# Performance work log

Hardware: AMD Instinct MI355X
Metric: run time of the kernel (lower is better)

## Reference

```python
import jax, jax.numpy as jnp
import numpy as np

D_K = 32
N_HEADS = 16


def setup_inputs() -> dict:
    key = jax.random.key(0)
    ks = jax.random.split(key, 11)
    B, S, F = 32, 2048, 128
    d_k, d_v, filt = 32, 32, 3
    return {
        "q_in": jax.random.normal(ks[0], (B, S, F), jnp.float32),
        "k_in": jax.random.normal(ks[1], (B, S, F), jnp.float32),
        "v_in": jax.random.normal(ks[2], (B, S, F), jnp.float32),
        "Wq": jax.random.normal(ks[3], (F, d_k), jnp.float32) * 0.05,
        "bq": jax.random.normal(ks[4], (d_k,), jnp.float32) * 0.05,
        "Wk": jax.random.normal(ks[5], (F, d_k), jnp.float32) * 0.05,
        "bk": jax.random.normal(ks[6], (d_k,), jnp.float32) * 0.05,
        "Wv": jax.random.normal(ks[7], (F, d_v), jnp.float32) * 0.05,
        "bv": jax.random.normal(ks[8], (d_v,), jnp.float32) * 0.05,
        "Wo": jax.random.normal(ks[9], (N_HEADS * d_v, filt), jnp.float32) * 0.05,
        "bo": jax.random.normal(ks[10], (filt,), jnp.float32) * 0.05,
    }


def reference(q_in, k_in, v_in, Wq, bq, Wk, bk, Wv, bv, Wo, bo):
    # SingleAttention: Dense projections then scaled dot-product attention.
    q = q_in @ Wq + bq            # [B,S,d_k]
    k = k_in @ Wk + bk            # [B,S,d_k]
    v = v_in @ Wv + bv            # [B,S,d_v]
    scores = jnp.einsum('bqd,bkd->bqk', q, k) / jnp.sqrt(jnp.float32(D_K))
    attn = jax.nn.softmax(scores, axis=-1)
    head = jnp.einsum('bqk,bkd->bqd', attn, v)  # [B,S,d_v]
    # Original uses [SingleAttention()]*n_heads -> all heads are the SAME layer,
    # so the concat is n_heads identical copies of one head output.
    combined = jnp.tile(head, (1, 1, N_HEADS))   # [B,S,n_heads*d_v]
    return combined @ Wo + bo                    # [B,S,filter_size]
```

## Files before the change

### kernel.cpp

```cpp
#include <hip/hip_runtime.h>
#include <stdint.h>

using f16 = _Float16;
typedef _Float16 f16x8 __attribute__((ext_vector_type(8)));
typedef float f32x4 __attribute__((ext_vector_type(4)));

constexpr int Bn    = 32;
constexpr int Sn    = 2048;
constexpr int Fn    = 128;
constexpr int DKn   = 32;
constexpr int NHn   = 16;
constexpr int FILTn = 3;
constexpr int Mn    = Bn * Sn;

constexpr float QSCALE = 0.1767766952966369f * 1.4426950408889634f;

constexpr int MISC_WOEFF = 0;
constexpr int MISC_BO    = 96;
constexpr int MISC_BQ    = 99;
constexpr int MISC_BK    = 131;
constexpr int MISC_BV    = 163;

#define ASYNC_COPY16(gp, lp)                                                   \
    __builtin_amdgcn_global_load_lds(                                          \
        (const __attribute__((address_space(1))) uint32_t*)(const void*)(gp),  \
        (__attribute__((address_space(3))) uint32_t*)(lp), 16, 0, 0)

#define WAIT_VM2 __builtin_amdgcn_s_waitcnt(0xF72)
#define WAIT_VM0 __builtin_amdgcn_s_waitcnt(0xF70)

__global__ __launch_bounds__(256) void prep_kernel(
    const float* __restrict__ Wq, const float* __restrict__ bq,
    const float* __restrict__ Wk, const float* __restrict__ bk,
    const float* __restrict__ Wv, const float* __restrict__ bv,
    const float* __restrict__ Wo, const float* __restrict__ bo,
    f16* __restrict__ wtg, float* __restrict__ misc)
{
    for (int idx = blockIdx.x * 256 + threadIdx.x; idx < 3 * 4096;
         idx += gridDim.x * 256) {
        const int T    = idx >> 12;
        const int r    = idx & 4095;
        const int nt   = r >> 11;
        const int ks   = (r >> 9) & 3;
        const int lane = (r >> 3) & 63;
        const int j    = r & 7;
        const int k    = ks * 32 + (lane >> 4) * 8 + j;
        const int c    = nt * 16 + (lane & 15);
        const float* W = (T == 0) ? Wq : ((T == 1) ? Wk : Wv);
        const float sc = (T == 0) ? QSCALE : 1.0f;
        wtg[idx] = (f16)(W[k * DKn + c] * sc);
    }
    if (blockIdx.x == 0) {
        const int t = threadIdx.x;
        if (t < 96) {
            const int d = t / 3, f = t - 3 * d;
            float s = 0.f;
#pragma unroll
            for (int h = 0; h < NHn; ++h) s += Wo[(h * DKn + d) * FILTn + f];
            misc[MISC_WOEFF + t] = s;
        } else if (t < 99) {
            misc[MISC_BO + (t - 96)] = bo[t - 96];
        } else if (t < 131) {
            misc[MISC_BQ + (t - 99)] = bq[t - 99] * QSCALE;
        } else if (t < 163) {
            misc[MISC_BK + (t - 131)] = bk[t - 131];
        } else if (t < 195) {
            misc[MISC_BV + (t - 163)] = bv[t - 163];
        }
    }
}

__global__ __launch_bounds__(256, 4) void qkv_proj(
    const float* __restrict__ q_in, const float* __restrict__ k_in,
    const float* __restrict__ v_in,
    const f16* __restrict__ wtg, const float* __restrict__ misc,
    f16* __restrict__ q_ws, f16* __restrict__ k_ws, f16* __restrict__ v_ws)
{
    const int t    = threadIdx.x;
    const int w    = t >> 6;
    const int lane = t & 63;
    const int n    = lane & 15;
    const int quad = lane >> 4;
    const int T    = blockIdx.x >> 10;
    const int row0 = ((blockIdx.x & 1023) * 4 + w) * 16;
    const float* in = (T == 0) ? q_in : ((T == 1) ? k_in : v_in);

    f16x8 wf[2][4];
#pragma unroll
    for (int nt = 0; nt < 2; ++nt)
#pragma unroll
        for (int ks = 0; ks < 4; ++ks)
            wf[nt][ks] =
                *(const f16x8*)(wtg + T * 4096 + (nt * 4 + ks) * 512 + lane * 8);

    f16x8 af[4];
#pragma unroll
    for (int ks = 0; ks < 4; ++ks) {
        const float* p  = in + (size_t)(row0 + n) * Fn + ks * 32 + quad * 8;
        const float4 x0 = *(const float4*)p;
        const float4 x1 = *(const float4*)(p + 4);
        f16x8 a;
        a[0]=(f16)x0.x; a[1]=(f16)x0.y; a[2]=(f16)x0.z; a[3]=(f16)x0.w;
        a[4]=(f16)x1.x; a[5]=(f16)x1.y; a[6]=(f16)x1.z; a[7]=(f16)x1.w;
        af[ks] = a;
    }

    if (T < 2) {
        const float* bb = misc + (T == 0 ? MISC_BQ : MISC_BK);
        const float b0 = bb[n], b1 = bb[16 + n];
        f32x4 acc0 = {b0, b0, b0, b0};
        f32x4 acc1 = {b1, b1, b1, b1};
#pragma unroll
        for (int ks = 0; ks < 4; ++ks) {
            acc0 = __builtin_amdgcn_mfma_f32_16x16x32_f16(af[ks], wf[0][ks], acc0, 0, 0, 0);
            acc1 = __builtin_amdgcn_mfma_f32_16x16x32_f16(af[ks], wf[1][ks], acc1, 0, 0, 0);
        }
        if (T == 0) {
#pragma unroll
            for (int r = 0; r < 4; ++r) {
                const int row = row0 + quad * 4 + r;
                q_ws[(size_t)row * DKn + n]      = (f16)acc0[r];
                q_ws[(size_t)row * DKn + 16 + n] = (f16)acc1[r];
            }
        } else {
#pragma unroll
            for (int r = 0; r < 4; ++r) {
                const int row = row0 + quad * 4 + r;
                const int b   = row >> 11;
                const int s   = row & (Sn - 1);
                const int kt  = s >> 6;
                const int key = s & 63;
                const size_t tbase = ((size_t)b * 32 + kt) * 2048;
                const int b16 = ((key >> 1) << 3) | ((key & 1) << 2);
                k_ws[tbase + (size_t)(b16 + (n >> 3)) * 8 + (n & 7)]     = (f16)acc0[r];
                k_ws[tbase + (size_t)(b16 + 2 + (n >> 3)) * 8 + (n & 7)] = (f16)acc1[r];
            }
        }
    } else {
        f32x4 acc0 = {0.f, 0.f, 0.f, 0.f};
        f32x4 acc1 = {0.f, 0.f, 0.f, 0.f};
#pragma unroll
        for (int ks = 0; ks < 4; ++ks) {
            acc0 = __builtin_amdgcn_mfma_f32_16x16x32_f16(wf[0][ks], af[ks], acc0, 0, 0, 0);
            acc1 = __builtin_amdgcn_mfma_f32_16x16x32_f16(wf[1][ks], af[ks], acc1, 0, 0, 0);
        }
        const int b  = row0 >> 11;
        const int s0 = (row0 & (Sn - 1)) + n;
#pragma unroll
        for (int r = 0; r < 4; ++r) {
            const int d0 = quad * 4 + r;
            v_ws[((size_t)(b * DKn + d0)) * Sn + s0] =
                (f16)(acc0[r] + misc[MISC_BV + d0]);
            v_ws[((size_t)(b * DKn + 16 + d0)) * Sn + s0] =
                (f16)(acc1[r] + misc[MISC_BV + 16 + d0]);
        }
    }
}

__global__ __launch_bounds__(256, 4) void flash_mfma(
    const f16* __restrict__ q_ws, const f16* __restrict__ k_ws,
    const f16* __restrict__ v_ws,
    const float* __restrict__ misc, float* __restrict__ out)
{
    __shared__ f16 kv[3][2][2048];
    __shared__ f16 psh[4 * 16 * 64];

    const int t    = threadIdx.x;
    const int w    = t >> 6;
    const int lane = t & 63;
    const int n    = lane & 15;
    const int quad = lane >> 4;
    const int b    = (blockIdx.x & 7) * 4 + (blockIdx.x >> 8);
    const int qt   = (blockIdx.x >> 3) & 31;

    const f16* Ktiles = k_ws + (size_t)b * Sn * DKn;
    const f16* Vbase  = v_ws + (size_t)b * DKn * Sn;

#define STAGE(KT, BUF)                                                          \
    {                                                                           \
        ASYNC_COPY16(Ktiles + (size_t)(KT) * 2048 + t * 8, &kv[BUF][0][w * 512]); \
        ASYNC_COPY16(Vbase + (size_t)(t >> 3) * Sn + (KT) * 64 + (t & 7) * 8,   \
                     &kv[BUF][1][w * 512]);                                     \
    }

    const int qrow0 = b * Sn + qt * 64 + w * 16;
    const f16x8 qa = *(const f16x8*)(q_ws + (size_t)(qrow0 + n) * DKn + quad * 8);

    int koff[4];
#pragma unroll
    for (int g = 0; g < 4; ++g)
        koff[g] = ((((g * 16 + n) >> 1) * 8 + (n & 1) * 4 + quad)) * 8;
    int voff[2][2];
#pragma unroll
    for (int ks = 0; ks < 2; ++ks) {
        voff[0][ks] = (n * 8 + ks * 4 + quad) * 8;
        voff[1][ks] = ((16 + n) * 8 + ks * 4 + quad) * 8;
    }

    f16* pw = psh + w * 16 * 64;
    const f16* prd0 = pw + n * 64 + ((quad ^ (n & 7)) << 3);
    const f16* prd1 = pw + n * 64 + (((4 + quad) ^ (n & 7)) << 3);
    int pwo[16];
#pragma unroll
    for (int r = 0; r < 4; ++r) {
        const int row = quad * 4 + r;
#pragma unroll
        for (int g = 0; g < 4; ++g)
            pwo[r * 4 + g] =
                row * 64 + (((g * 2 + (n >> 3)) ^ (row & 7)) << 3) + (n & 7);
    }

    f32x4 o0 = {0.f, 0.f, 0.f, 0.f};
    f32x4 o1 = {0.f, 0.f, 0.f, 0.f};
    float l[4] = {0.f, 0.f, 0.f, 0.f};
    const f32x4 zero = {0.f, 0.f, 0.f, 0.f};

    STAGE(0, 0)
    STAGE(1, 1)

#pragma unroll 1
    for (int kt = 0; kt < Sn / 64; ++kt) {
        const int cur = kt % 3;
        WAIT_VM2;
        __builtin_amdgcn_s_barrier();
        STAGE((kt + 2) & 31, (kt + 2) % 3)

        const f16* Kt = &kv[cur][0][0];
        const f16* Vt = &kv[cur][1][0];

        const f16x8 kb0 = *(const f16x8*)(Kt + koff[0]);
        const f16x8 kb1 = *(const f16x8*)(Kt + koff[1]);
        const f16x8 kb2 = *(const f16x8*)(Kt + koff[2]);
        const f16x8 kb3 = *(const f16x8*)(Kt + koff[3]);
        const f16x8 va0 = *(const f16x8*)(Vt + voff[0][0]);
        const f16x8 va1 = *(const f16x8*)(Vt + voff[0][1]);
        const f16x8 va2 = *(const f16x8*)(Vt + voff[1][0]);
        const f16x8 va3 = *(const f16x8*)(Vt + voff[1][1]);

        const f32x4 s0 = __builtin_amdgcn_mfma_f32_16x16x32_f16(qa, kb0, zero, 0, 0, 0);
        const f32x4 s1 = __builtin_amdgcn_mfma_f32_16x16x32_f16(qa, kb1, zero, 0, 0, 0);
        const f32x4 s2 = __builtin_amdgcn_mfma_f32_16x16x32_f16(qa, kb2, zero, 0, 0, 0);
        const f32x4 s3 = __builtin_amdgcn_mfma_f32_16x16x32_f16(qa, kb3, zero, 0, 0, 0);

#pragma unroll
        for (int r = 0; r < 4; ++r) {
            const float p0 = __builtin_amdgcn_exp2f(s0[r]);
            const float p1 = __builtin_amdgcn_exp2f(s1[r]);
            const float p2 = __builtin_amdgcn_exp2f(s2[r]);
            const float p3 = __builtin_amdgcn_exp2f(s3[r]);
            l[r] += (p0 + p1) + (p2 + p3);
            pw[pwo[r * 4 + 0]] = (f16)p0;
            pw[pwo[r * 4 + 1]] = (f16)p1;
            pw[pwo[r * 4 + 2]] = (f16)p2;
            pw[pwo[r * 4 + 3]] = (f16)p3;
        }

        const f16x8 pa0 = *(const f16x8*)prd0;
        const f16x8 pa1 = *(const f16x8*)prd1;
        o0 = __builtin_amdgcn_mfma_f32_16x16x32_f16(pa0, va0, o0, 0, 0, 0);
        o0 = __builtin_amdgcn_mfma_f32_16x16x32_f16(pa1, va1, o0, 0, 0, 0);
        o1 = __builtin_amdgcn_mfma_f32_16x16x32_f16(pa0, va2, o1, 0, 0, 0);
        o1 = __builtin_amdgcn_mfma_f32_16x16x32_f16(pa1, va3, o1, 0, 0, 0);
    }
#undef STAGE
    WAIT_VM0;

#pragma unroll
    for (int r = 0; r < 4; ++r) {
        float v = l[r];
        v += __shfl_xor(v, 1, 16);
        v += __shfl_xor(v, 2, 16);
        v += __shfl_xor(v, 4, 16);
        v += __shfl_xor(v, 8, 16);
        l[r] = v;
    }

    float w0f[FILTn], w1f[FILTn];
#pragma unroll
    for (int f = 0; f < FILTn; ++f) {
        w0f[f] = misc[MISC_WOEFF + n * FILTn + f];
        w1f[f] = misc[MISC_WOEFF + (16 + n) * FILTn + f];
    }
#pragma unroll
    for (int r = 0; r < 4; ++r) {
        const float inv = 1.f / l[r];
        const float a0 = o0[r] * inv;
        const float a1 = o1[r] * inv;
#pragma unroll
        for (int f = 0; f < FILTn; ++f) {
            float v = a0 * w0f[f] + a1 * w1f[f];
            v += __shfl_xor(v, 1, 16);
            v += __shfl_xor(v, 2, 16);
            v += __shfl_xor(v, 4, 16);
            v += __shfl_xor(v, 8, 16);
            if (n == f) {
                const int row = qrow0 + quad * 4 + r;
                out[(size_t)row * FILTn + f] = v + misc[MISC_BO + f];
            }
        }
    }
}

extern "C" void kernel_launch(void* const* d_in, const int* in_sizes, int n_in,
                              void* d_out, int out_size, void* d_ws,
                              size_t ws_size, hipStream_t stream)
{
    const float* q_in = (const float*)d_in[0];
    const float* k_in = (const float*)d_in[1];
    const float* v_in = (const float*)d_in[2];
    const float* Wq   = (const float*)d_in[3];
    const float* bq   = (const float*)d_in[4];
    const float* Wk   = (const float*)d_in[5];
    const float* bk   = (const float*)d_in[6];
    const float* Wv   = (const float*)d_in[7];
    const float* bv   = (const float*)d_in[8];
    const float* Wo   = (const float*)d_in[9];
    const float* bo   = (const float*)d_in[10];
    float* out = (float*)d_out;

    f16*   ws   = (f16*)d_ws;
    f16*   q_ws = ws;
    f16*   k_ws = ws + (size_t)Mn * DKn;
    f16*   v_ws = ws + 2 * (size_t)Mn * DKn;
    f16*   wtg  = ws + 3 * (size_t)Mn * DKn;
    float* misc = (float*)(wtg + 3 * 4096);

    prep_kernel<<<16, 256, 0, stream>>>(Wq, bq, Wk, bk, Wv, bv, Wo, bo, wtg, misc);

    qkv_proj<<<3 * 1024, 256, 0, stream>>>(
        q_in, k_in, v_in, wtg, misc, q_ws, k_ws, v_ws);

    flash_mfma<<<Bn * (Sn / 64), 256, 0, stream>>>(
        q_ws, k_ws, v_ws, misc, out);
}
```

Baseline: 195.2 us.

## Process two row tiles per wave in projection and swizzle K/V LDS layout

The projection kernel now has each wave compute two 16-row tiles, halving the grid and reusing the loaded weight fragments across twice as many MFMAs. K is written in plain row-major order instead of a pre-tiled layout. The attention kernel's async copies apply an XOR swizzle on the global source side, with matching read offsets, to avoid LDS bank conflicts. This trades more registers and fewer blocks in the projection for fewer weight reloads and simpler, conflict-free K/V staging.

Result: faster. 185.8 us (-4.8%).

```diff
diff --git a/kernel.cpp b/kernel.cpp
--- a/kernel.cpp
+++ b/kernel.cpp
@@ -70,7 +70,7 @@
     }
 }
 
-__global__ __launch_bounds__(256, 4) void qkv_proj(
+__global__ __launch_bounds__(256) void qkv_proj(
     const float* __restrict__ q_in, const float* __restrict__ k_in,
     const float* __restrict__ v_in,
     const f16* __restrict__ wtg, const float* __restrict__ misc,
@@ -81,8 +81,9 @@
     const int lane = t & 63;
     const int n    = lane & 15;
     const int quad = lane >> 4;
-    const int T    = blockIdx.x >> 10;
-    const int row0 = ((blockIdx.x & 1023) * 4 + w) * 16;
+    const int T    = blockIdx.x / 512;
+    const int rowA = (((blockIdx.x - T * 512) * 4 + w)) * 32;
+    const int rowB = rowA + 16;
     const float* in = (T == 0) ? q_in : ((T == 1) ? k_in : v_in);
 
     f16x8 wf[2][4];
@@ -93,66 +94,70 @@
             wf[nt][ks] =
                 *(const f16x8*)(wtg + T * 4096 + (nt * 4 + ks) * 512 + lane * 8);
 
-    f16x8 af[4];
+    f16x8 afA[4], afB[4];
 #pragma unroll
     for (int ks = 0; ks < 4; ++ks) {
-        const float* p  = in + (size_t)(row0 + n) * Fn + ks * 32 + quad * 8;
-        const float4 x0 = *(const float4*)p;
-        const float4 x1 = *(const float4*)(p + 4);
-        f16x8 a;
-        a[0]=(f16)x0.x; a[1]=(f16)x0.y; a[2]=(f16)x0.z; a[3]=(f16)x0.w;
-        a[4]=(f16)x1.x; a[5]=(f16)x1.y; a[6]=(f16)x1.z; a[7]=(f16)x1.w;
-        af[ks] = a;
+        const float* pA = in + (size_t)(rowA + n) * Fn + ks * 32 + quad * 8;
+        const float* pB = in + (size_t)(rowB + n) * Fn + ks * 32 + quad * 8;
+        const float4 a0 = *(const float4*)pA;
+        const float4 a1 = *(const float4*)(pA + 4);
+        const float4 b0 = *(const float4*)pB;
+        const float4 b1 = *(const float4*)(pB + 4);
+        f16x8 a, b;
+        a[0]=(f16)a0.x; a[1]=(f16)a0.y; a[2]=(f16)a0.z; a[3]=(f16)a0.w;
+        a[4]=(f16)a1.x; a[5]=(f16)a1.y; a[6]=(f16)a1.z; a[7]=(f16)a1.w;
+        b[0]=(f16)b0.x; b[1]=(f16)b0.y; b[2]=(f16)b0.z; b[3]=(f16)b0.w;
+        b[4]=(f16)b1.x; b[5]=(f16)b1.y; b[6]=(f16)b1.z; b[7]=(f16)b1.w;
+        afA[ks] = a;
+        afB[ks] = b;
     }
 
     if (T < 2) {
         const float* bb = misc + (T == 0 ? MISC_BQ : MISC_BK);
         const float b0 = bb[n], b1 = bb[16 + n];
-        f32x4 acc0 = {b0, b0, b0, b0};
-        f32x4 acc1 = {b1, b1, b1, b1};
+        f32x4 accA0 = {b0, b0, b0, b0}, accA1 = {b1, b1, b1, b1};
+        f32x4 accB0 = {b0, b0, b0, b0}, accB1 = {b1, b1, b1, b1};
 #pragma unroll
         for (int ks = 0; ks < 4; ++ks) {
-            acc0 = __builtin_amdgcn_mfma_f32_16x16x32_f16(af[ks], wf[0][ks], acc0, 0, 0, 0);
-            acc1 = __builtin_amdgcn_mfma_f32_16x16x32_f16(af[ks], wf[1][ks], acc1, 0, 0, 0);
-        }
-        if (T == 0) {
-#pragma unroll
-            for (int r = 0; r < 4; ++r) {
-                const int row = row0 + quad * 4 + r;
-                q_ws[(size_t)row * DKn + n]      = (f16)acc0[r];
-                q_ws[(size_t)row * DKn + 16 + n] = (f16)acc1[r];
-            }
-        } else {
-#pragma unroll
-            for (int r = 0; r < 4; ++r) {
-                const int row = row0 + quad * 4 + r;
-                const int b   = row >> 11;
-                const int s   = row & (Sn - 1);
-                const int kt  = s >> 6;
-                const int key = s & 63;
-                const size_t tbase = ((size_t)b * 32 + kt) * 2048;
-                const int b16 = ((key >> 1) << 3) | ((key & 1) << 2);
-                k_ws[tbase + (size_t)(b16 + (n >> 3)) * 8 + (n & 7)]     = (f16)acc0[r];
-                k_ws[tbase + (size_t)(b16 + 2 + (n >> 3)) * 8 + (n & 7)] = (f16)acc1[r];
-            }
+            accA0 = __builtin_amdgcn_mfma_f32_16x16x32_f16(afA[ks], wf[0][ks], accA0, 0, 0, 0);
+            accA1 = __builtin_amdgcn_mfma_f32_16x16x32_f16(afA[ks], wf[1][ks], accA1, 0, 0, 0);
+            accB0 = __builtin_amdgcn_mfma_f32_16x16x32_f16(afB[ks], wf[0][ks], accB0, 0, 0, 0);
+            accB1 = __builtin_amdgcn_mfma_f32_16x16x32_f16(afB[ks], wf[1][ks], accB1, 0, 0, 0);
+        }
+        f16* ows = (T == 0) ? q_ws : k_ws;
+#pragma unroll
+        for (int r = 0; r < 4; ++r) {
+            const int ra = rowA + quad * 4 + r;
+            const int rb = rowB + quad * 4 + r;
+            ows[(size_t)ra * DKn + n]      = (f16)accA0[r];
+            ows[(size_t)ra * DKn + 16 + n] = (f16)accA1[r];
+            ows[(size_t)rb * DKn + n]      = (f16)accB0[r];
+            ows[(size_t)rb * DKn + 16 + n] = (f16)accB1[r];
         }
     } else {
-        f32x4 acc0 = {0.f, 0.f, 0.f, 0.f};
-        f32x4 acc1 = {0.f, 0.f, 0.f, 0.f};
+        f32x4 accA0 = {0.f,0.f,0.f,0.f}, accA1 = {0.f,0.f,0.f,0.f};
+        f32x4 accB0 = {0.f,0.f,0.f,0.f}, accB1 = {0.f,0.f,0.f,0.f};
 #pragma unroll
         for (int ks = 0; ks < 4; ++ks) {
-            acc0 = __builtin_amdgcn_mfma_f32_16x16x32_f16(wf[0][ks], af[ks], acc0, 0, 0, 0);
-            acc1 = __builtin_amdgcn_mfma_f32_16x16x32_f16(wf[1][ks], af[ks], acc1, 0, 0, 0);
-        }
-        const int b  = row0 >> 11;
-        const int s0 = (row0 & (Sn - 1)) + n;
+            accA0 = __builtin_amdgcn_mfma_f32_16x16x32_f16(wf[0][ks], afA[ks], accA0, 0, 0, 0);
+            accA1 = __builtin_amdgcn_mfma_f32_16x16x32_f16(wf[1][ks], afA[ks], accA1, 0, 0, 0);
+            accB0 = __builtin_amdgcn_mfma_f32_16x16x32_f16(wf[0][ks], afB[ks], accB0, 0, 0, 0);
+            accB1 = __builtin_amdgcn_mfma_f32_16x16x32_f16(wf[1][ks], afB[ks], accB1, 0, 0, 0);
+        }
+        const int b  = rowA >> 11;
+        const int sA = (rowA & (Sn - 1)) + n;
+        const int sB = sA + 16;
 #pragma unroll
         for (int r = 0; r < 4; ++r) {
             const int d0 = quad * 4 + r;
-            v_ws[((size_t)(b * DKn + d0)) * Sn + s0] =
-                (f16)(acc0[r] + misc[MISC_BV + d0]);
-            v_ws[((size_t)(b * DKn + 16 + d0)) * Sn + s0] =
-                (f16)(acc1[r] + misc[MISC_BV + 16 + d0]);
+            v_ws[((size_t)(b * DKn + d0)) * Sn + sA] =
+                (f16)(accA0[r] + misc[MISC_BV + d0]);
+            v_ws[((size_t)(b * DKn + 16 + d0)) * Sn + sA] =
+                (f16)(accA1[r] + misc[MISC_BV + 16 + d0]);
+            v_ws[((size_t)(b * DKn + d0)) * Sn + sB] =
+                (f16)(accB0[r] + misc[MISC_BV + d0]);
+            v_ws[((size_t)(b * DKn + 16 + d0)) * Sn + sB] =
+                (f16)(accB1[r] + misc[MISC_BV + 16 + d0]);
         }
     }
 }
@@ -173,14 +178,15 @@
     const int b    = (blockIdx.x & 7) * 4 + (blockIdx.x >> 8);
     const int qt   = (blockIdx.x >> 3) & 31;
 
-    const f16* Ktiles = k_ws + (size_t)b * Sn * DKn;
-    const f16* Vbase  = v_ws + (size_t)b * DKn * Sn;
-
-#define STAGE(KT, BUF)                                                          \
-    {                                                                           \
-        ASYNC_COPY16(Ktiles + (size_t)(KT) * 2048 + t * 8, &kv[BUF][0][w * 512]); \
-        ASYNC_COPY16(Vbase + (size_t)(t >> 3) * Sn + (KT) * 64 + (t & 7) * 8,   \
-                     &kv[BUF][1][w * 512]);                                     \
+    const f16* Ksrc = k_ws + (size_t)b * Sn * DKn
+                    + (size_t)(t >> 2) * DKn + (((t & 3) ^ ((t >> 3) & 3)) * 8);
+    const f16* Vsrc = v_ws + (size_t)b * DKn * Sn
+                    + (size_t)(t >> 3) * Sn + (((t & 7) ^ ((t >> 3) & 7)) * 8);
+
+#define STAGE(KT, BUF)                                              \
+    {                                                               \
+        ASYNC_COPY16(Ksrc + (size_t)(KT) * 2048, &kv[BUF][0][w * 512]); \
+        ASYNC_COPY16(Vsrc + (size_t)(KT) * 64,   &kv[BUF][1][w * 512]); \
     }
 
     const int qrow0 = b * Sn + qt * 64 + w * 16;
@@ -189,12 +195,12 @@
     int koff[4];
 #pragma unroll
     for (int g = 0; g < 4; ++g)
-        koff[g] = ((((g * 16 + n) >> 1) * 8 + (n & 1) * 4 + quad)) * 8;
+        koff[g] = (g * 64 + n * 4 + (quad ^ ((n >> 1) & 3))) * 8;
     int voff[2][2];
 #pragma unroll
     for (int ks = 0; ks < 2; ++ks) {
-        voff[0][ks] = (n * 8 + ks * 4 + quad) * 8;
-        voff[1][ks] = ((16 + n) * 8 + ks * 4 + quad) * 8;
+        voff[0][ks] = (n * 8 + ((ks * 4 + quad) ^ (n & 7))) * 8;
+        voff[1][ks] = ((16 + n) * 8 + ((ks * 4 + quad) ^ (n & 7))) * 8;
     }
 
     f16* pw = psh + w * 16 * 64;
@@ -327,7 +333,7 @@
 
     prep_kernel<<<16, 256, 0, stream>>>(Wq, bq, Wk, bk, Wv, bv, Wo, bo, wtg, misc);
 
-    qkv_proj<<<3 * 1024, 256, 0, stream>>>(
+    qkv_proj<<<3 * 512, 256, 0, stream>>>(
         q_in, k_in, v_in, wtg, misc, q_ws, k_ws, v_ws);
 
     flash_mfma<<<Bn * (Sn / 64), 256, 0, stream>>>(
```
